# Performance work log

Measured on AMD Instinct MI355X. Metric: run time of the kernel, lower is better.

Reference implementation:

```python
import jax, jax.numpy as jnp
import numpy as np

L, D, H, FF, P, IMG, B = 6, 1024, 16, 4096, 14, 224, 16
S = (IMG // P) ** 2 + 1  # 257 tokens (CLS + patches)
DH = D // H
TOPK_RATIO, MOD_START, MOD_END = 0.8, 3, -2
EPS = 1e-5


def _ln(x, w, b):
    m = x.mean(-1, keepdims=True)
    v = ((x - m) ** 2).mean(-1, keepdims=True)
    return (x - m) * jax.lax.rsqrt(v + EPS) * w + b


def _quick_gelu(x):
    return x * jax.nn.sigmoid(1.702 * x)


def setup_inputs() -> dict:
    key = jax.random.key(0)
    ks = jax.random.split(key, 16)
    w = 0.02
    inp = {
        "pixel_values": jax.random.normal(ks[0], (B, 3, IMG, IMG), jnp.float32),
        "patch_w": jax.random.normal(ks[1], (D, 3, P, P), jnp.float32) * w,
        "class_emb": jax.random.normal(ks[2], (D,), jnp.float32) * w,
        "pos_emb": jax.random.normal(ks[3], (S, D), jnp.float32) * w,
        "ln1_w": jnp.ones((L, D), jnp.float32),
        "ln1_b": jnp.zeros((L, D), jnp.float32),
        "q_w": jax.random.normal(ks[4], (L, D, D), jnp.float32) * w,
        "q_b": jnp.zeros((L, D), jnp.float32),
        "k_w": jax.random.normal(ks[5], (L, D, D), jnp.float32) * w,
        "k_b": jnp.zeros((L, D), jnp.float32),
        "v_w": jax.random.normal(ks[6], (L, D, D), jnp.float32) * w,
        "v_b": jnp.zeros((L, D), jnp.float32),
        "o_w": jax.random.normal(ks[7], (L, D, D), jnp.float32) * w,
        "o_b": jnp.zeros((L, D), jnp.float32),
        "ln2_w": jnp.ones((L, D), jnp.float32),
        "ln2_b": jnp.zeros((L, D), jnp.float32),
        "fc1_w": jax.random.normal(ks[8], (L, FF, D), jnp.float32) * w,
        "fc1_b": jnp.zeros((L, FF), jnp.float32),
        "fc2_w": jax.random.normal(ks[9], (L, D, FF), jnp.float32) * w,
        "fc2_b": jnp.zeros((L, D), jnp.float32),
    }
    return inp


def reference(pixel_values, patch_w, class_emb, pos_emb,
              ln1_w, ln1_b, q_w, q_b, k_w, k_b, v_w, v_b, o_w, o_b,
              ln2_w, ln2_b, fc1_w, fc1_b, fc2_w, fc2_b):
    # --- CLIP vision embeddings (note: custom forward skips pre_layrnorm) ---
    feats = jax.lax.conv_general_dilated(
        pixel_values, patch_w, (P, P), 'VALID',
        dimension_numbers=('NCHW', 'OIHW', 'NCHW'))  # [B, D, 16, 16]
    feats = feats.reshape(B, D, -1).transpose(0, 2, 1)  # [B, 256, D]
    cls = jnp.broadcast_to(class_emb, (B, 1, D))
    x = jnp.concatenate([cls, feats], axis=1) + pos_emb[None]  # [B, S, D]

    scale = DH ** -0.5
    top_k = int(S * TOPK_RATIO)

    for idx in range(L):
        # --- CLIP encoder layer (pre-LN) ---
        res = x
        h = _ln(x, ln1_w[idx], ln1_b[idx])
        q = (h @ q_w[idx].T + q_b[idx]).reshape(B, S, H, DH)
        k = (h @ k_w[idx].T + k_b[idx]).reshape(B, S, H, DH)
        v = (h @ v_w[idx].T + v_b[idx]).reshape(B, S, H, DH)
        scores = jnp.einsum('bqhd,bkhd->bhqk', q, k) * scale
        attn = jax.nn.softmax(scores, axis=-1)  # [B, H, S, S]
        ctx = jnp.einsum('bhqk,bkhd->bqhd', attn, v).reshape(B, S, D)
        x = res + (ctx @ o_w[idx].T + o_b[idx])
        res = x
        h = _ln(x, ln2_w[idx], ln2_b[idx])
        h = _quick_gelu(h @ fc1_w[idx].T + fc1_b[idx])
        x = res + (h @ fc2_w[idx].T + fc2_b[idx])

        # --- MoD-style top-k selection + per-batch mask scatter ---
        if MOD_START <= idx <= L + MOD_END and (idx - MOD_START) % 2 == 0:
            aw = attn.mean(axis=1)                 # [B, S, S]
            sc = aw.sum(axis=2)                    # [B, S]
            sc = sc / sc.sum(axis=1, keepdims=True)
            _, top_idx = jax.lax.top_k(sc, top_k)  # [B, top_k]
            mask = jnp.zeros((B, S), bool).at[jnp.arange(B)[:, None], top_idx].set(True)
            # Original torch loop writes hidden_states back into a clone on both
            # mask and ~mask -> mathematically an identity copy.
            x = jnp.where(mask[:, :, None], x, x)

    return x


if __name__ == '__main__':
    out = reference(**setup_inputs())
    print(out.shape, out.dtype)
```

## Files before the change

### kernel.cpp

```cpp
#include <hip/hip_runtime.h>
#include <stdint.h>

typedef uint16_t u16;
typedef __attribute__((ext_vector_type(8))) short short8;
typedef __attribute__((ext_vector_type(4))) float f32x4;
typedef __attribute__((ext_vector_type(4))) u16 u16x4;

__device__ __forceinline__ u16 f2bf(float f) {
  union { float f; uint32_t i; } v; v.f = f;
  uint32_t r = v.i + 0x7fffu + ((v.i >> 16) & 1u);
  return (u16)(r >> 16);
}
__device__ __forceinline__ int imin(int a, int b) { return a < b ? a : b; }

#define GLD_LDS(gp, lp) __builtin_amdgcn_global_load_lds( \
    (__attribute__((address_space(1))) void*)(uintptr_t)(gp), \
    (__attribute__((address_space(3))) void*)(lp), 16, 0, 0)

#define BATCH 16
#define SEQ 257
#define DIM 1024
#define HEADS 16
#define DHEAD 64
#define FFDIM 4096
#define MROWS (BATCH * SEQ)
#define SPAD 288
#define KC 608

enum { EPI_PATCH = 0, EPI_QK = 1, EPI_VT = 2, EPI_RES = 3, EPI_GELU = 4 };

struct GemmP {
  const u16* A; const u16* B;
  const float* bias;
  int lda, ldb, M, N, K;
  void* out;
  const float* aux;
};

template <int EPI>
__global__ __launch_bounds__(256) void gemm_bt(GemmP p) {
  __shared__ __align__(16) u16 sA[128 * 32];
  __shared__ __align__(16) u16 sB[128 * 32];
  const int tid = threadIdx.x;
  const int w = tid >> 6, l = tid & 63, quad = l >> 4, lr = l & 15;
  const int wr = w >> 1, wc = w & 1;
  const int m0 = blockIdx.y * 128, n0 = blockIdx.x * 128;
  const u16* A = p.A;
  const u16* B = p.B;

  const int f0 = tid, f1 = tid + 256;
  const int ar0 = f0 >> 2, as0 = f0 & 3, ar1 = f1 >> 2, as1 = f1 & 3;
  const long aoff0 = (long)imin(m0 + ar0, p.M - 1) * p.lda + (as0 << 3);
  const long aoff1 = (long)imin(m0 + ar1, p.M - 1) * p.lda + (as1 << 3);
  const long boff0 = (long)imin(n0 + ar0, p.N - 1) * p.ldb + (as0 << 3);
  const long boff1 = (long)imin(n0 + ar1, p.N - 1) * p.ldb + (as1 << 3);

  f32x4 acc[4][4];
#pragma unroll
  for (int i = 0; i < 4; ++i)
#pragma unroll
    for (int j = 0; j < 4; ++j) acc[i][j] = (f32x4){0.f, 0.f, 0.f, 0.f};

  for (int k0 = 0; k0 < p.K; k0 += 32) {
    __syncthreads();
    GLD_LDS(A + aoff0 + k0, &sA[f0 * 8]);
    GLD_LDS(A + aoff1 + k0, &sA[f1 * 8]);
    GLD_LDS(B + boff0 + k0, &sB[f0 * 8]);
    GLD_LDS(B + boff1 + k0, &sB[f1 * 8]);
    __syncthreads();
    short8 af[4], bg[4];
#pragma unroll
    for (int t = 0; t < 4; ++t) {
      af[t] = *(const short8*)&sA[(wr * 64 + t * 16 + lr) * 32 + quad * 8];
      bg[t] = *(const short8*)&sB[(wc * 64 + t * 16 + lr) * 32 + quad * 8];
    }
#pragma unroll
    for (int mt = 0; mt < 4; ++mt)
#pragma unroll
      for (int nt = 0; nt < 4; ++nt)
        acc[mt][nt] = __builtin_amdgcn_mfma_f32_16x16x32_bf16(af[mt], bg[nt], acc[mt][nt], 0, 0, 0);
  }

#pragma unroll
  for (int mt = 0; mt < 4; ++mt) {
#pragma unroll
    for (int r = 0; r < 4; ++r) {
      const int gm = m0 + wr * 64 + mt * 16 + quad * 4 + r;
      if (gm >= p.M) continue;
#pragma unroll
      for (int nt = 0; nt < 4; ++nt) {
        const int gn = n0 + wc * 64 + nt * 16 + lr;
        if (gn >= p.N) continue;
        float v = acc[mt][nt][r];
        if (p.bias) v += p.bias[gn];
        if constexpr (EPI == EPI_PATCH) {
          const int b = gm >> 8, pp = gm & 255;
          ((float*)p.out)[((long)(b * SEQ + 1 + pp)) * DIM + gn] =
              v + p.aux[(1 + pp) * DIM + gn];
        } else if constexpr (EPI == EPI_QK) {
          const int b = gm / SEQ, s = gm % SEQ;
          const int h = gn >> 6, d = gn & 63;
          ((u16*)p.out)[(((long)(b * HEADS + h) * SEQ + s)) * DHEAD + d] = f2bf(v);
        } else if constexpr (EPI == EPI_VT) {
          const int b = gm / SEQ, s = gm % SEQ;
          const int h = gn >> 6, d = gn & 63;
          ((u16*)p.out)[((long)(b * HEADS + h) * DHEAD + d) * SPAD + s] = f2bf(v);
        } else if constexpr (EPI == EPI_RES) {
          float* o = (float*)p.out;
          o[(long)gm * p.N + gn] += v;
        } else if constexpr (EPI == EPI_GELU) {
          const float g = v / (1.f + __expf(-1.702f * v));
          ((u16*)p.out)[(long)gm * p.N + gn] = f2bf(g);
        }
      }
    }
  }
}

__global__ __launch_bounds__(256) void ln_k(const float* __restrict__ X,
                                            const float* __restrict__ w,
                                            const float* __restrict__ b,
                                            u16* __restrict__ O) {
  const int row = blockIdx.x, tid = threadIdx.x;
  const float4* xr = (const float4*)(X + (long)row * DIM);
  float4 v = xr[tid];
  float s = v.x + v.y + v.z + v.w;
  float s2 = v.x * v.x + v.y * v.y + v.z * v.z + v.w * v.w;
  for (int o = 32; o; o >>= 1) { s += __shfl_xor(s, o); s2 += __shfl_xor(s2, o); }
  __shared__ float red[8];
  const int wv = tid >> 6, l = tid & 63;
  if (l == 0) { red[wv] = s; red[4 + wv] = s2; }
  __syncthreads();
  s = red[0] + red[1] + red[2] + red[3];
  s2 = red[4] + red[5] + red[6] + red[7];
  const float mean = s * (1.f / DIM);
  const float var = s2 * (1.f / DIM) - mean * mean;
  const float rs = rsqrtf(var + 1e-5f);
  const int c = tid * 4;
  const float4 wv4 = *(const float4*)(w + c);
  const float4 bv4 = *(const float4*)(b + c);
  u16x4 o4;
  o4.x = f2bf((v.x - mean) * rs * wv4.x + bv4.x);
  o4.y = f2bf((v.y - mean) * rs * wv4.y + bv4.y);
  o4.z = f2bf((v.z - mean) * rs * wv4.z + bv4.z);
  o4.w = f2bf((v.w - mean) * rs * wv4.w + bv4.w);
  *(u16x4*)(O + (long)row * DIM + c) = o4;
}

__global__ __launch_bounds__(256) void attn_k(const u16* __restrict__ Q,
                                              const u16* __restrict__ Kx,
                                              const u16* __restrict__ Vt,
                                              u16* __restrict__ Ctx) {
  const int bh = blockIdx.x;
  const int q0 = blockIdx.y * 16;
  __shared__ float S[16][292];
  __shared__ __align__(16) u16 P[16][SPAD];
  const int tid = threadIdx.x, w = tid >> 6, l = tid & 63, quad = l >> 4, lr = l & 15;
  const u16* Qb = Q + (long)bh * SEQ * DHEAD;
  const u16* Kb = Kx + (long)bh * SEQ * DHEAD;
  const u16* Vb = Vt + (long)bh * DHEAD * SPAD;
  int qm = q0 + lr; if (qm > SEQ - 1) qm = SEQ - 1;
  const short8 aq0 = *(const short8*)(Qb + qm * DHEAD + quad * 8);
  const short8 aq1 = *(const short8*)(Qb + qm * DHEAD + 32 + quad * 8);
  for (int ct = 0; ct < 5; ++ct) {
    const int cn = ct * 64 + w * 16 + lr;
    const int cc = cn > SEQ - 1 ? SEQ - 1 : cn;
    const short8 b0 = *(const short8*)(Kb + cc * DHEAD + quad * 8);
    const short8 b1 = *(const short8*)(Kb + cc * DHEAD + 32 + quad * 8);
    f32x4 acc = (f32x4){0.f, 0.f, 0.f, 0.f};
    acc = __builtin_amdgcn_mfma_f32_16x16x32_bf16(aq0, b0, acc, 0, 0, 0);
    acc = __builtin_amdgcn_mfma_f32_16x16x32_bf16(aq1, b1, acc, 0, 0, 0);
    if (cn < SEQ) {
#pragma unroll
      for (int r = 0; r < 4; ++r) S[quad * 4 + r][cn] = acc[r] * 0.125f;
    }
  }
  __syncthreads();
#pragma unroll
  for (int rr = 0; rr < 4; ++rr) {
    const int m = w * 4 + rr;
    float mx = -1e30f;
    for (int c = l; c < SEQ; c += 64) mx = fmaxf(mx, S[m][c]);
    for (int o = 32; o; o >>= 1) mx = fmaxf(mx, __shfl_xor(mx, o));
    float sum = 0.f;
    for (int c = l; c < SEQ; c += 64) {
      const float e = __expf(S[m][c] - mx);
      S[m][c] = e;
      sum += e;
    }
    for (int o = 32; o; o >>= 1) sum += __shfl_xor(sum, o);
    const float inv = 1.f / sum;
    for (int c = l; c < SPAD; c += 64) P[m][c] = (c < SEQ) ? f2bf(S[m][c] * inv) : (u16)0;
  }
  __syncthreads();
  f32x4 acc = (f32x4){0.f, 0.f, 0.f, 0.f};
  for (int k0 = 0; k0 < SPAD; k0 += 32) {
    const short8 ap = *(const short8*)&P[lr][k0 + quad * 8];
    const short8 bv = *(const short8*)(Vb + (long)(w * 16 + lr) * SPAD + k0 + quad * 8);
    acc = __builtin_amdgcn_mfma_f32_16x16x32_bf16(ap, bv, acc, 0, 0, 0);
  }
  const int b = bh >> 4, h = bh & 15;
#pragma unroll
  for (int r = 0; r < 4; ++r) {
    const int q = q0 + quad * 4 + r;
    if (q < SEQ)
      Ctx[((long)(b * SEQ + q)) * DIM + h * DHEAD + w * 16 + lr] = f2bf(acc[r]);
  }
}

__global__ void f2b_k(const float* __restrict__ src, u16* __restrict__ dst, int n4) {
  const int i = blockIdx.x * 256 + threadIdx.x;
  if (i >= n4) return;
  const float4 v = ((const float4*)src)[i];
  u16x4 o;
  o.x = f2bf(v.x); o.y = f2bf(v.y); o.z = f2bf(v.z); o.w = f2bf(v.w);
  ((u16x4*)dst)[i] = o;
}

__global__ void im2col_k(const float* __restrict__ pv, u16* __restrict__ out) {
  const long i = (long)blockIdx.x * 256 + threadIdx.x;
  if (i >= (long)4096 * KC) return;
  const int col = (int)(i % KC);
  const long row = i / KC;
  u16 val = 0;
  if (col < 588) {
    const int b = (int)(row >> 8), p = (int)(row & 255);
    const int py = p >> 4, px = p & 15;
    const int c = col / 196, rem = col % 196;
    const int ky = rem / 14, kx = rem % 14;
    val = f2bf(pv[(((long)b * 3 + c) * 224 + (py * 14 + ky)) * 224 + (px * 14 + kx)]);
  }
  out[i] = val;
}

__global__ void pwpad_k(const float* __restrict__ pw, u16* __restrict__ out) {
  const int i = blockIdx.x * 256 + threadIdx.x;
  if (i >= DIM * KC) return;
  const int col = i % KC, row = i / KC;
  out[i] = (col < 588) ? f2bf(pw[row * 588 + col]) : (u16)0;
}

__global__ void cls_k(const float* __restrict__ cls, const float* __restrict__ pos,
                      float* __restrict__ X) {
  const int i = blockIdx.x * 256 + threadIdx.x;
  const int b = i >> 10, d = i & 1023;
  X[((long)b * SEQ) * DIM + d] = cls[d] + pos[d];
}

__global__ void vtpad_k(u16* __restrict__ Vt) {
  const int i = blockIdx.x * 256 + threadIdx.x;
  if (i >= 256 * 64 * 31) return;
  const int dall = i / 31, s = SEQ + i % 31;
  Vt[(long)dall * SPAD + s] = 0;
}

__global__ void out_k(const float* __restrict__ X, float* __restrict__ O) {
  const int i = blockIdx.x * 256 + threadIdx.x;
  ((float4*)O)[i] = ((const float4*)X)[i];
}

#define OFF_X 0L
#define OFF_H 16842752L
#define OFF_Q 25264128L
#define OFF_K 33685504L
#define OFF_VT 42106880L
#define OFF_CTX 51544064L
#define OFF_FF 59965440L
#define OFF_W 93650944L
#define OFF_IM OFF_FF
#define OFF_PW (OFF_FF + 4980736L)

extern "C" void kernel_launch(void* const* d_in, const int* in_sizes, int n_in,
                              void* d_out, int out_size, void* d_ws, size_t ws_size,
                              hipStream_t stream) {
  const float* pv = (const float*)d_in[0];
  const float* patch_w = (const float*)d_in[1];
  const float* class_emb = (const float*)d_in[2];
  const float* pos_emb = (const float*)d_in[3];
  const float* ln1_w = (const float*)d_in[4];
  const float* ln1_b = (const float*)d_in[5];
  const float* q_w = (const float*)d_in[6];
  const float* q_b = (const float*)d_in[7];
  const float* k_w = (const float*)d_in[8];
  const float* k_b = (const float*)d_in[9];
  const float* v_w = (const float*)d_in[10];
  const float* v_b = (const float*)d_in[11];
  const float* o_w = (const float*)d_in[12];
  const float* o_b = (const float*)d_in[13];
  const float* ln2_w = (const float*)d_in[14];
  const float* ln2_b = (const float*)d_in[15];
  const float* fc1_w = (const float*)d_in[16];
  const float* fc1_b = (const float*)d_in[17];
  const float* fc2_w = (const float*)d_in[18];
  const float* fc2_b = (const float*)d_in[19];

  char* ws = (char*)d_ws;
  float* X = (float*)(ws + OFF_X);
  u16* Hb = (u16*)(ws + OFF_H);
  u16* Qb = (u16*)(ws + OFF_Q);
  u16* Kb = (u16*)(ws + OFF_K);
  u16* Vt = (u16*)(ws + OFF_VT);
  u16* Ctx = (u16*)(ws + OFF_CTX);
  u16* FFh = (u16*)(ws + OFF_FF);
  u16* Wb = (u16*)(ws + OFF_W);
  u16* Im = (u16*)(ws + OFF_IM);
  u16* Pw = (u16*)(ws + OFF_PW);

  const int NSQ4 = DIM * DIM / 4;
  const int NFF4 = FFDIM * DIM / 4;
  const int GSQ = (NSQ4 + 255) / 256, GFF = (NFF4 + 255) / 256;

  im2col_k<<<(4096 * KC + 255) / 256, 256, 0, stream>>>(pv, Im);
  pwpad_k<<<(DIM * KC + 255) / 256, 256, 0, stream>>>(patch_w, Pw);
  cls_k<<<(BATCH * DIM) / 256, 256, 0, stream>>>(class_emb, pos_emb, X);
  vtpad_k<<<(256 * 64 * 31 + 255) / 256, 256, 0, stream>>>(Vt);
  {
    GemmP g = {};
    g.A = Im; g.lda = KC; g.B = Pw; g.ldb = KC; g.bias = nullptr;
    g.M = 4096; g.N = DIM; g.K = KC; g.out = X; g.aux = pos_emb;
    gemm_bt<EPI_PATCH><<<dim3(8, 32, 1), 256, 0, stream>>>(g);
  }

  for (int idx = 0; idx < 6; ++idx) {
    ln_k<<<MROWS, 256, 0, stream>>>(X, ln1_w + idx * DIM, ln1_b + idx * DIM, Hb);
    {
      GemmP g = {};
      g.A = Hb; g.lda = DIM; g.B = Wb; g.ldb = DIM;
      g.M = MROWS; g.N = DIM; g.K = DIM;
      f2b_k<<<GSQ, 256, 0, stream>>>(q_w + (long)idx * DIM * DIM, Wb, NSQ4);
      g.bias = q_b + idx * DIM; g.out = Qb;
      gemm_bt<EPI_QK><<<dim3(8, 33, 1), 256, 0, stream>>>(g);
      f2b_k<<<GSQ, 256, 0, stream>>>(k_w + (long)idx * DIM * DIM, Wb, NSQ4);
      g.bias = k_b + idx * DIM; g.out = Kb;
      gemm_bt<EPI_QK><<<dim3(8, 33, 1), 256, 0, stream>>>(g);
      f2b_k<<<GSQ, 256, 0, stream>>>(v_w + (long)idx * DIM * DIM, Wb, NSQ4);
      g.bias = v_b + idx * DIM; g.out = Vt;
      gemm_bt<EPI_VT><<<dim3(8, 33, 1), 256, 0, stream>>>(g);
    }
    attn_k<<<dim3(256, 17, 1), 256, 0, stream>>>(Qb, Kb, Vt, Ctx);
    {
      GemmP g = {};
      f2b_k<<<GSQ, 256, 0, stream>>>(o_w + (long)idx * DIM * DIM, Wb, NSQ4);
      g.A = Ctx; g.lda = DIM; g.B = Wb; g.ldb = DIM;
      g.bias = o_b + idx * DIM; g.M = MROWS; g.N = DIM; g.K = DIM; g.out = X;
      gemm_bt<EPI_RES><<<dim3(8, 33, 1), 256, 0, stream>>>(g);
    }
    ln_k<<<MROWS, 256, 0, stream>>>(X, ln2_w + idx * DIM, ln2_b + idx * DIM, Hb);
    {
      GemmP g = {};
      f2b_k<<<GFF, 256, 0, stream>>>(fc1_w + (long)idx * FFDIM * DIM, Wb, NFF4);
      g.A = Hb; g.lda = DIM; g.B = Wb; g.ldb = DIM;
      g.bias = fc1_b + idx * FFDIM; g.M = MROWS; g.N = FFDIM; g.K = DIM; g.out = FFh;
      gemm_bt<EPI_GELU><<<dim3(32, 33, 1), 256, 0, stream>>>(g);
    }
    {
      GemmP g = {};
      f2b_k<<<GFF, 256, 0, stream>>>(fc2_w + (long)idx * DIM * FFDIM, Wb, NFF4);
      g.A = FFh; g.lda = FFDIM; g.B = Wb; g.ldb = FFDIM;
      g.bias = fc2_b + idx * DIM; g.M = MROWS; g.N = DIM; g.K = FFDIM; g.out = X;
      gemm_bt<EPI_RES><<<dim3(8, 33, 1), 256, 0, stream>>>(g);
    }
  }
  out_k<<<(MROWS * DIM / 4) / 256, 256, 0, stream>>>(X, (float*)d_out);
}
```

Before: 3.106 ms.

## Fuse Q/K/V projections into one GEMM and use smaller M tiles for N=1024 GEMMs

Converts the Q, K and V weights into one contiguous bf16 buffer with a concatenated bias, then runs a single GEMM with N=3072 whose epilogue routes each column segment to the Q, K or transposed V output. The GEMM template gains an M-tile parameter, and the patch, out-projection and fc2 GEMMs switch to 64-row tiles. This doubles their block count so a 256-CU device is better filled. Fusing QKV removes two launches and gives more blocks per wave. Smaller tiles lower per-block reuse of the B operand.

```diff
diff --git a/kernel.cpp b/kernel.cpp
--- a/kernel.cpp
+++ b/kernel.cpp
@@ -27,65 +27,75 @@
 #define SPAD 288
 #define KC 608
 
-enum { EPI_PATCH = 0, EPI_QK = 1, EPI_VT = 2, EPI_RES = 3, EPI_GELU = 4 };
+enum { EPI_PATCH = 0, EPI_QKV = 1, EPI_RES = 2, EPI_GELU = 3 };
 
 struct GemmP {
   const u16* A; const u16* B;
   const float* bias;
   int lda, ldb, M, N, K;
   void* out;
+  void* out2; void* out3;
   const float* aux;
 };
 
-template <int EPI>
+template <int EPI, int MT>
 __global__ __launch_bounds__(256) void gemm_bt(GemmP p) {
-  __shared__ __align__(16) u16 sA[128 * 32];
+  constexpr int TM = MT * 32;
+  constexpr int AISS = MT / 2;
+  __shared__ __align__(16) u16 sA[TM * 32];
   __shared__ __align__(16) u16 sB[128 * 32];
   const int tid = threadIdx.x;
   const int w = tid >> 6, l = tid & 63, quad = l >> 4, lr = l & 15;
   const int wr = w >> 1, wc = w & 1;
-  const int m0 = blockIdx.y * 128, n0 = blockIdx.x * 128;
-  const u16* A = p.A;
-  const u16* B = p.B;
-
-  const int f0 = tid, f1 = tid + 256;
-  const int ar0 = f0 >> 2, as0 = f0 & 3, ar1 = f1 >> 2, as1 = f1 & 3;
-  const long aoff0 = (long)imin(m0 + ar0, p.M - 1) * p.lda + (as0 << 3);
-  const long aoff1 = (long)imin(m0 + ar1, p.M - 1) * p.lda + (as1 << 3);
-  const long boff0 = (long)imin(n0 + ar0, p.N - 1) * p.ldb + (as0 << 3);
-  const long boff1 = (long)imin(n0 + ar1, p.N - 1) * p.ldb + (as1 << 3);
-
-  f32x4 acc[4][4];
-#pragma unroll
-  for (int i = 0; i < 4; ++i)
+  const int m0 = blockIdx.y * TM, n0 = blockIdx.x * 128;
+
+  long aoff[AISS];
+#pragma unroll
+  for (int i = 0; i < AISS; ++i) {
+    const int f = tid + i * 256;
+    aoff[i] = (long)imin(m0 + (f >> 2), p.M - 1) * p.lda + ((f & 3) << 3);
+  }
+  long boff[2];
+#pragma unroll
+  for (int i = 0; i < 2; ++i) {
+    const int f = tid + i * 256;
+    boff[i] = (long)imin(n0 + (f >> 2), p.N - 1) * p.ldb + ((f & 3) << 3);
+  }
+
+  f32x4 acc[MT][4];
+#pragma unroll
+  for (int i = 0; i < MT; ++i)
 #pragma unroll
     for (int j = 0; j < 4; ++j) acc[i][j] = (f32x4){0.f, 0.f, 0.f, 0.f};
 
   for (int k0 = 0; k0 < p.K; k0 += 32) {
     __syncthreads();
-    GLD_LDS(A + aoff0 + k0, &sA[f0 * 8]);
-    GLD_LDS(A + aoff1 + k0, &sA[f1 * 8]);
-    GLD_LDS(B + boff0 + k0, &sB[f0 * 8]);
-    GLD_LDS(B + boff1 + k0, &sB[f1 * 8]);
+#pragma unroll
+    for (int i = 0; i < AISS; ++i)
+      GLD_LDS(p.A + aoff[i] + k0, &sA[(tid + i * 256) * 8]);
+#pragma unroll
+    for (int i = 0; i < 2; ++i)
+      GLD_LDS(p.B + boff[i] + k0, &sB[(tid + i * 256) * 8]);
     __syncthreads();
-    short8 af[4], bg[4];
-#pragma unroll
-    for (int t = 0; t < 4; ++t) {
-      af[t] = *(const short8*)&sA[(wr * 64 + t * 16 + lr) * 32 + quad * 8];
+    short8 af[MT], bg[4];
+#pragma unroll
+    for (int t = 0; t < MT; ++t)
+      af[t] = *(const short8*)&sA[(wr * (MT * 16) + t * 16 + lr) * 32 + quad * 8];
+#pragma unroll
+    for (int t = 0; t < 4; ++t)
       bg[t] = *(const short8*)&sB[(wc * 64 + t * 16 + lr) * 32 + quad * 8];
-    }
-#pragma unroll
-    for (int mt = 0; mt < 4; ++mt)
+#pragma unroll
+    for (int mt = 0; mt < MT; ++mt)
 #pragma unroll
       for (int nt = 0; nt < 4; ++nt)
         acc[mt][nt] = __builtin_amdgcn_mfma_f32_16x16x32_bf16(af[mt], bg[nt], acc[mt][nt], 0, 0, 0);
   }
 
 #pragma unroll
-  for (int mt = 0; mt < 4; ++mt) {
+  for (int mt = 0; mt < MT; ++mt) {
 #pragma unroll
     for (int r = 0; r < 4; ++r) {
-      const int gm = m0 + wr * 64 + mt * 16 + quad * 4 + r;
+      const int gm = m0 + wr * (MT * 16) + mt * 16 + quad * 4 + r;
       if (gm >= p.M) continue;
 #pragma unroll
       for (int nt = 0; nt < 4; ++nt) {
@@ -97,14 +107,17 @@
           const int b = gm >> 8, pp = gm & 255;
           ((float*)p.out)[((long)(b * SEQ + 1 + pp)) * DIM + gn] =
               v + p.aux[(1 + pp) * DIM + gn];
-        } else if constexpr (EPI == EPI_QK) {
+        } else if constexpr (EPI == EPI_QKV) {
           const int b = gm / SEQ, s = gm % SEQ;
-          const int h = gn >> 6, d = gn & 63;
-          ((u16*)p.out)[(((long)(b * HEADS + h) * SEQ + s)) * DHEAD + d] = f2bf(v);
-        } else if constexpr (EPI == EPI_VT) {
-          const int b = gm / SEQ, s = gm % SEQ;
-          const int h = gn >> 6, d = gn & 63;
-          ((u16*)p.out)[((long)(b * HEADS + h) * DHEAD + d) * SPAD + s] = f2bf(v);
+          const int seg = gn >> 10, dloc = gn & 1023;
+          const int h = dloc >> 6, dd = dloc & 63;
+          const u16 val = f2bf(v);
+          if (seg == 0)
+            ((u16*)p.out)[(((long)(b * HEADS + h) * SEQ + s)) * DHEAD + dd] = val;
+          else if (seg == 1)
+            ((u16*)p.out2)[(((long)(b * HEADS + h) * SEQ + s)) * DHEAD + dd] = val;
+          else
+            ((u16*)p.out3)[((long)(b * HEADS + h) * DHEAD + dd) * SPAD + s] = val;
         } else if constexpr (EPI == EPI_RES) {
           float* o = (float*)p.out;
           o[(long)gm * p.N + gn] += v;
@@ -217,6 +230,12 @@
   ((u16x4*)dst)[i] = o;
 }
 
+__global__ void cat3_k(const float* __restrict__ a, const float* __restrict__ b,
+                       const float* __restrict__ c, float* __restrict__ o) {
+  const int i = blockIdx.x * 256 + threadIdx.x;
+  o[i] = (i < 1024) ? a[i] : (i < 2048 ? b[i - 1024] : c[i - 2048]);
+}
+
 __global__ void im2col_k(const float* __restrict__ pv, u16* __restrict__ out) {
   const long i = (long)blockIdx.x * 256 + threadIdx.x;
   if (i >= (long)4096 * KC) return;
@@ -267,6 +286,7 @@
 #define OFF_CTX 51544064L
 #define OFF_FF 59965440L
 #define OFF_W 93650944L
+#define OFF_B3 (OFF_W + 6291456L)
 #define OFF_IM OFF_FF
 #define OFF_PW (OFF_FF + 4980736L)
 
@@ -303,6 +323,7 @@
   u16* Ctx = (u16*)(ws + OFF_CTX);
   u16* FFh = (u16*)(ws + OFF_FF);
   u16* Wb = (u16*)(ws + OFF_W);
+  float* B3 = (float*)(ws + OFF_B3);
   u16* Im = (u16*)(ws + OFF_IM);
   u16* Pw = (u16*)(ws + OFF_PW);
 
@@ -318,24 +339,21 @@
     GemmP g = {};
     g.A = Im; g.lda = KC; g.B = Pw; g.ldb = KC; g.bias = nullptr;
     g.M = 4096; g.N = DIM; g.K = KC; g.out = X; g.aux = pos_emb;
-    gemm_bt<EPI_PATCH><<<dim3(8, 32, 1), 256, 0, stream>>>(g);
+    gemm_bt<EPI_PATCH, 2><<<dim3(8, 64, 1), 256, 0, stream>>>(g);
   }
 
   for (int idx = 0; idx < 6; ++idx) {
     ln_k<<<MROWS, 256, 0, stream>>>(X, ln1_w + idx * DIM, ln1_b + idx * DIM, Hb);
     {
+      f2b_k<<<GSQ, 256, 0, stream>>>(q_w + (long)idx * DIM * DIM, Wb, NSQ4);
+      f2b_k<<<GSQ, 256, 0, stream>>>(k_w + (long)idx * DIM * DIM, Wb + DIM * DIM, NSQ4);
+      f2b_k<<<GSQ, 256, 0, stream>>>(v_w + (long)idx * DIM * DIM, Wb + 2 * DIM * DIM, NSQ4);
+      cat3_k<<<12, 256, 0, stream>>>(q_b + idx * DIM, k_b + idx * DIM, v_b + idx * DIM, B3);
       GemmP g = {};
-      g.A = Hb; g.lda = DIM; g.B = Wb; g.ldb = DIM;
-      g.M = MROWS; g.N = DIM; g.K = DIM;
-      f2b_k<<<GSQ, 256, 0, stream>>>(q_w + (long)idx * DIM * DIM, Wb, NSQ4);
-      g.bias = q_b + idx * DIM; g.out = Qb;
-      gemm_bt<EPI_QK><<<dim3(8, 33, 1), 256, 0, stream>>>(g);
-      f2b_k<<<GSQ, 256, 0, stream>>>(k_w + (long)idx * DIM * DIM, Wb, NSQ4);
-      g.bias = k_b + idx * DIM; g.out = Kb;
-      gemm_bt<EPI_QK><<<dim3(8, 33, 1), 256, 0, stream>>>(g);
-      f2b_k<<<GSQ, 256, 0, stream>>>(v_w + (long)idx * DIM * DIM, Wb, NSQ4);
-      g.bias = v_b + idx * DIM; g.out = Vt;
-      gemm_bt<EPI_VT><<<dim3(8, 33, 1), 256, 0, stream>>>(g);
+      g.A = Hb; g.lda = DIM; g.B = Wb; g.ldb = DIM; g.bias = B3;
+      g.M = MROWS; g.N = 3 * DIM; g.K = DIM;
+      g.out = Qb; g.out2 = Kb; g.out3 = Vt;
+      gemm_bt<EPI_QKV, 4><<<dim3(24, 33, 1), 256, 0, stream>>>(g);
     }
     attn_k<<<dim3(256, 17, 1), 256, 0, stream>>>(Qb, Kb, Vt, Ctx);
     {
@@ -343,7 +361,7 @@
       f2b_k<<<GSQ, 256, 0, stream>>>(o_w + (long)idx * DIM * DIM, Wb, NSQ4);
       g.A = Ctx; g.lda = DIM; g.B = Wb; g.ldb = DIM;
       g.bias = o_b + idx * DIM; g.M = MROWS; g.N = DIM; g.K = DIM; g.out = X;
-      gemm_bt<EPI_RES><<<dim3(8, 33, 1), 256, 0, stream>>>(g);
+      gemm_bt<EPI_RES, 2><<<dim3(8, 65, 1), 256, 0, stream>>>(g);
     }
     ln_k<<<MROWS, 256, 0, stream>>>(X, ln2_w + idx * DIM, ln2_b + idx * DIM, Hb);
     {
@@ -351,14 +369,14 @@
       f2b_k<<<GFF, 256, 0, stream>>>(fc1_w + (long)idx * FFDIM * DIM, Wb, NFF4);
       g.A = Hb; g.lda = DIM; g.B = Wb; g.ldb = DIM;
       g.bias = fc1_b + idx * FFDIM; g.M = MROWS; g.N = FFDIM; g.K = DIM; g.out = FFh;
-      gemm_bt<EPI_GELU><<<dim3(32, 33, 1), 256, 0, stream>>>(g);
+      gemm_bt<EPI_GELU, 4><<<dim3(32, 33, 1), 256, 0, stream>>>(g);
     }
     {
       GemmP g = {};
       f2b_k<<<GFF, 256, 0, stream>>>(fc2_w + (long)idx * DIM * FFDIM, Wb, NFF4);
       g.A = FFh; g.lda = FFDIM; g.B = Wb; g.ldb = FFDIM;
       g.bias = fc2_b + idx * DIM; g.M = MROWS; g.N = DIM; g.K = FFDIM; g.out = X;
-      gemm_bt<EPI_RES><<<dim3(8, 33, 1), 256, 0, stream>>>(g);
+      gemm_bt<EPI_RES, 2><<<dim3(8, 65, 1), 256, 0, stream>>>(g);
     }
   }
   out_k<<<(MROWS * DIM / 4) / 256, 256, 0, stream>>>(X, (float*)d_out);
```

Measured after the change: 2.571 ms. -17.2%, faster.
